# Kernel optimization log

Hardware: AMD Instinct MI355X
Metric: run time of the kernel (lower is better)

## Reference

```python
import jax, jax.numpy as jnp
import numpy as np

N_NODES = 100000


def gcn_conv(x, src, dst, W, b, n_nodes):
    """PyG GCNConv: out = D^{-1/2} (A + I) D^{-1/2} X W + b (self-loops added)."""
    h = x @ W  # [N, out]
    loops = jnp.arange(n_nodes, dtype=src.dtype)
    s = jnp.concatenate([src, loops])
    d = jnp.concatenate([dst, loops])
    deg = jax.ops.segment_sum(jnp.ones_like(d, dtype=h.dtype), d, num_segments=n_nodes)
    dinv = jnp.where(deg > 0, jax.lax.rsqrt(deg), 0.0)
    norm = dinv[s] * dinv[d]  # [E+N]
    msgs = norm[:, None] * h[s]  # gather + scale
    out = jax.ops.segment_sum(msgs, d, num_segments=n_nodes)
    return out + b


def setup_inputs() -> dict:
    key = jax.random.key(0)
    ks = jax.random.split(key, 10)
    n, e, f_in = N_NODES, 1600000, 128
    x = jax.random.normal(ks[0], (n, f_in), dtype=jnp.float32)
    edge_index = jax.random.randint(ks[1], (2, e), 0, n, dtype=jnp.int64)
    dims = [f_in, 15, 20, 27, 36]
    params = {}
    for i in range(4):
        fan_in, fan_out = dims[i], dims[i + 1]
        scale = 1.0 / np.sqrt(fan_in)
        params[f"W{i+1}"] = jax.random.uniform(ks[2 + 2 * i], (fan_in, fan_out), minval=-scale, maxval=scale, dtype=jnp.float32)
        params[f"b{i+1}"] = jax.random.uniform(ks[3 + 2 * i], (fan_out,), minval=-scale, maxval=scale, dtype=jnp.float32)
    return {"x": x, "edge_index": edge_index, **params}


def reference(x, edge_index, W1, b1, W2, b2, W3, b3, W4, b4):
    src, dst = edge_index[0], edge_index[1]
    n = x.shape[0]
    h = jax.nn.selu(gcn_conv(x, src, dst, W1, b1, n))
    h = jax.nn.selu(gcn_conv(h, src, dst, W2, b2, n))
    h = jax.nn.selu(gcn_conv(h, src, dst, W3, b3, n))
    h = jax.nn.selu(gcn_conv(h, src, dst, W4, b4, n))
    return h
```

## Files before the change

kernel.cpp:

```cpp
#include <hip/hip_runtime.h>
#include <hip/hip_fp16.h>
#include <math.h>

#define BLK 256
#define CBSH 10
#define CBN 1024
#define NCBC 128
#define NB2 512

__device__ __forceinline__ float selu_f(float x) {
    const float kScale = 1.0507009873554805f;
    const float kAlpha = 1.6732632423543772f;
    return x > 0.0f ? kScale * x : kScale * kAlpha * expm1f(x);
}

__device__ __forceinline__ float2 h2f2(unsigned u) {
    __half2 h = *reinterpret_cast<__half2*>(&u);
    return __half22float2(h);
}
__device__ __forceinline__ void h8_set(float* a, uint4 v) {
    float2 f0 = h2f2(v.x), f1 = h2f2(v.y), f2 = h2f2(v.z), f3 = h2f2(v.w);
    a[0] = f0.x; a[1] = f0.y; a[2] = f1.x; a[3] = f1.y;
    a[4] = f2.x; a[5] = f2.y; a[6] = f3.x; a[7] = f3.y;
}
__device__ __forceinline__ void h8_add(float* a, uint4 v) {
    float2 f0 = h2f2(v.x), f1 = h2f2(v.y), f2 = h2f2(v.z), f3 = h2f2(v.w);
    a[0] += f0.x; a[1] += f0.y; a[2] += f1.x; a[3] += f1.y;
    a[4] += f2.x; a[5] += f2.y; a[6] += f3.x; a[7] += f3.y;
}

__global__ void k_cnt(const int* __restrict__ dst, int* __restrict__ H, int e, int nbkt) {
    __shared__ int hist[NCBC];
    int tid = threadIdx.x;
    for (int b = tid; b < nbkt; b += BLK) hist[b] = 0;
    __syncthreads();
    int per = (e + NB2 - 1) / NB2;
    int lo = blockIdx.x * per;
    int hi = min(e, lo + per);
    for (int i = lo + tid; i < hi; i += BLK) atomicAdd(&hist[dst[i] >> CBSH], 1);
    __syncthreads();
    for (int b = tid; b < nbkt; b += BLK) H[blockIdx.x * nbkt + b] = hist[b];
}

__global__ void k_bsum(const int* __restrict__ H, int* __restrict__ bstart, int nbkt, int e) {
    __shared__ int tot[NCBC];
    int tid = threadIdx.x;
    for (int b = tid; b < nbkt; b += BLK) {
        int s = 0;
        for (int i = 0; i < NB2; ++i) s += H[i * nbkt + b];
        tot[b] = s;
    }
    __syncthreads();
    if (tid == 0) {
        int acc = 0;
        for (int b = 0; b < nbkt; ++b) {
            bstart[b] = acc;
            acc += tot[b];
        }
        bstart[nbkt] = acc;
    }
}

__global__ void k_off(int* __restrict__ H, const int* __restrict__ bstart, int nbkt) {
    __shared__ int lds[BLK];
    int b = blockIdx.x, tid = threadIdx.x;
    int v0 = H[(2 * tid) * nbkt + b];
    int v1 = H[(2 * tid + 1) * nbkt + b];
    int pair = v0 + v1;
    lds[tid] = pair;
    __syncthreads();
    int val = pair;
    for (int off = 1; off < BLK; off <<= 1) {
        int t2 = (tid >= off) ? lds[tid - off] : 0;
        __syncthreads();
        val += t2;
        lds[tid] = val;
        __syncthreads();
    }
    int excl = val - pair + bstart[b];
    H[(2 * tid) * nbkt + b] = excl;
    H[(2 * tid + 1) * nbkt + b] = excl + v0;
}

__global__ void k_scatter2(const int* __restrict__ src, const int* __restrict__ dst,
                           const int* __restrict__ H, unsigned* __restrict__ slab,
                           int e, int nbkt) {
    __shared__ int cur[NCBC];
    int tid = threadIdx.x;
    for (int b = tid; b < nbkt; b += BLK) cur[b] = H[blockIdx.x * nbkt + b];
    __syncthreads();
    int per = (e + NB2 - 1) / NB2;
    int lo = blockIdx.x * per;
    int hi = min(e, lo + per);
    for (int i = lo + tid; i < hi; i += BLK) {
        int s = src[i], d = dst[i];
        int b = d >> CBSH;
        int pos = atomicAdd(&cur[b], 1);
        slab[pos] = ((unsigned)s << CBSH) | (unsigned)(d & (CBN - 1));
    }
}

__global__ void k_histB(const int* __restrict__ bstart, const unsigned* __restrict__ slab,
                        int* __restrict__ deg, int n) {
    __shared__ int hist[CBN];
    int b = blockIdx.x, tid = threadIdx.x;
    for (int j = tid; j < CBN; j += BLK) hist[j] = 0;
    __syncthreads();
    int lo = bstart[b], hi = bstart[b + 1];
    for (int i = lo + tid; i < hi; i += BLK) atomicAdd(&hist[slab[i] & (CBN - 1)], 1);
    __syncthreads();
    int node0 = b << CBSH;
    for (int j = tid; j < CBN; j += BLK) {
        int node = node0 + j;
        if (node < n) deg[node] = hist[j];
    }
}

__global__ void k_scan1(const int* __restrict__ deg, int* __restrict__ rowptr,
                        int* __restrict__ bsums, int n) {
    __shared__ int lds[BLK];
    int tid = threadIdx.x;
    int idx = blockIdx.x * (BLK * 4) + tid * 4;
    int v0 = 0, v1 = 0, v2 = 0, v3 = 0;
    if (idx + 3 < n) {
        int4 t = *reinterpret_cast<const int4*>(deg + idx);
        v0 = t.x; v1 = t.y; v2 = t.z; v3 = t.w;
    } else {
        if (idx < n) v0 = deg[idx];
        if (idx + 1 < n) v1 = deg[idx + 1];
        if (idx + 2 < n) v2 = deg[idx + 2];
        if (idx + 3 < n) v3 = deg[idx + 3];
    }
    int tot = v0 + v1 + v2 + v3;
    lds[tid] = tot;
    __syncthreads();
    int val = tot;
    for (int off = 1; off < BLK; off <<= 1) {
        int t2 = (tid >= off) ? lds[tid - off] : 0;
        __syncthreads();
        val += t2;
        lds[tid] = val;
        __syncthreads();
    }
    int excl = val - tot;
    if (idx < n) rowptr[idx] = excl;
    if (idx + 1 < n) rowptr[idx + 1] = excl + v0;
    if (idx + 2 < n) rowptr[idx + 2] = excl + v0 + v1;
    if (idx + 3 < n) rowptr[idx + 3] = excl + v0 + v1 + v2;
    if (tid == BLK - 1) bsums[blockIdx.x] = val;
}

__global__ void k_scan2(int* __restrict__ bsums, int nb) {
    __shared__ int lds[BLK];
    int tid = threadIdx.x;
    int v = (tid < nb) ? bsums[tid] : 0;
    lds[tid] = v;
    __syncthreads();
    int val = v;
    for (int off = 1; off < BLK; off <<= 1) {
        int t2 = (tid >= off) ? lds[tid - off] : 0;
        __syncthreads();
        val += t2;
        lds[tid] = val;
        __syncthreads();
    }
    if (tid < nb) bsums[tid] = val - v;
}

__global__ void k_scan3(int* __restrict__ rowptr, const int* __restrict__ bsums,
                        const int* __restrict__ deg, float* __restrict__ dinv,
                        int n, int e) {
    int i = blockIdx.x * BLK + threadIdx.x;
    if (i >= n) return;
    int r = rowptr[i] + bsums[i >> 10];
    rowptr[i] = r;
    dinv[i] = rsqrtf((float)(deg[i] + 1));
    if (i == n - 1) rowptr[n] = e;
}

__global__ void k_placeC(const int* __restrict__ bstart, const unsigned* __restrict__ slab,
                         const int* __restrict__ rowptr, int* __restrict__ csr, int n) {
    __shared__ int cur[CBN];
    int b = blockIdx.x, tid = threadIdx.x;
    int node0 = b << CBSH;
    for (int j = tid; j < CBN; j += BLK) {
        int node = node0 + j;
        cur[j] = (node < n) ? rowptr[node] : 0;
    }
    __syncthreads();
    int lo = bstart[b], hi = bstart[b + 1];
    for (int i = lo + tid; i < hi; i += BLK) {
        unsigned p = slab[i];
        int pos = atomicAdd(&cur[p & (CBN - 1)], 1);
        csr[pos] = (int)(p >> CBSH);
    }
}

template <int K, int KP, int F, int SI, int SO, bool FUSE_IN>
__global__ void k_gemm(const float* __restrict__ xin, const float* __restrict__ W,
                       const float* __restrict__ bprev, const float* __restrict__ dinv,
                       __half* __restrict__ hs, int n) {
    constexpr int F8 = (F + 7) & ~7;
    int i = blockIdx.x * BLK + threadIdx.x;
    if (i >= n) return;
    const float* xr = xin + (size_t)i * SI;
    float di = dinv[i];
    float accf[F8];
#pragma unroll
    for (int f = 0; f < F8; ++f) accf[f] = 0.0f;
#pragma unroll
    for (int k4 = 0; k4 < KP / 4; ++k4) {
        float4 xv = *reinterpret_cast<const float4*>(xr + k4 * 4);
        float xs4[4] = {xv.x, xv.y, xv.z, xv.w};
#pragma unroll
        for (int j = 0; j < 4; ++j) {
            const int k = k4 * 4 + j;
            if (k < K) {
                float xval = xs4[j];
                if (FUSE_IN) xval = selu_f(di * xval + bprev[k]);
#pragma unroll
                for (int f = 0; f < F; ++f) accf[f] = fmaf(xval, W[k * F + f], accf[f]);
            }
        }
    }
#pragma unroll
    for (int f = 0; f < F; ++f) accf[f] *= di;
    __half2* ro2 = reinterpret_cast<__half2*>(hs + (size_t)i * SO);
#pragma unroll
    for (int f2 = 0; f2 < F8 / 2; ++f2)
        ro2[f2] = __float22half2_rn(make_float2(accf[2 * f2], accf[2 * f2 + 1]));
}

template <int F, int S , int G, int SOUT, bool LAST>
__global__ void k_agg(const int* __restrict__ rowptr, const int* __restrict__ csr,
                      const __half* __restrict__ hs, float* __restrict__ out,
                      const float* __restrict__ dinv, const float* __restrict__ bias,
                      int n) {
    constexpr int NPW = 64 / G;
    constexpr int CH = ((F + 7) & ~7) / 8;
    int lane = threadIdx.x & 63;
    int g = lane / G;
    int fl = lane & (G - 1);
    int wid = (blockIdx.x * BLK + threadIdx.x) >> 6;
    int d = wid * NPW + g;
    if (d >= n || fl >= CH) return;
    int beg = rowptr[d], end = rowptr[d + 1];
    auto rowp = [&](int r) {
        return reinterpret_cast<const uint4*>(hs + (size_t)r * S) + fl;
    };
    float s0[8], s1[8] = {0}, s2[8] = {0}, s3[8] = {0};
    h8_set(s0, *rowp(d));
    int p = beg;
    for (; p + 4 <= end; p += 4) {
        int e0 = csr[p], e1 = csr[p + 1], e2 = csr[p + 2], e3 = csr[p + 3];
        uint4 v0 = *rowp(e0), v1 = *rowp(e1), v2 = *rowp(e2), v3 = *rowp(e3);
        h8_add(s0, v0); h8_add(s1, v1); h8_add(s2, v2); h8_add(s3, v3);
    }
    for (; p < end; ++p) h8_add(s0, *rowp(csr[p]));
    float sum[8];
#pragma unroll
    for (int j = 0; j < 8; ++j) sum[j] = (s0[j] + s1[j]) + (s2[j] + s3[j]);
    if (LAST) {
        float dv = dinv[d];
        float r[8];
#pragma unroll
        for (int j = 0; j < 8; ++j) {
            int col = fl * 8 + j;
            r[j] = (col < F) ? selu_f(dv * sum[j] + bias[col]) : 0.0f;
        }
        float* op = out + (size_t)d * F + fl * 8;
        *reinterpret_cast<float4*>(op) = make_float4(r[0], r[1], r[2], r[3]);
        if (fl * 8 + 4 < F)
            *reinterpret_cast<float4*>(op + 4) = make_float4(r[4], r[5], r[6], r[7]);
    } else {
        float* op = out + (size_t)d * SOUT + fl * 8;
        *reinterpret_cast<float4*>(op) = make_float4(sum[0], sum[1], sum[2], sum[3]);
        *reinterpret_cast<float4*>(op + 4) = make_float4(sum[4], sum[5], sum[6], sum[7]);
    }
}

extern "C" void kernel_launch(void* const* d_in, const int* in_sizes, int n_in,
                              void* d_out, int out_size, void* d_ws, size_t ws_size,
                              hipStream_t stream) {
    const float* x = (const float*)d_in[0];
    const int* ei = (const int*)d_in[1];
    const float* W1 = (const float*)d_in[2];
    const float* b1 = (const float*)d_in[3];
    const float* W2 = (const float*)d_in[4];
    const float* b2 = (const float*)d_in[5];
    const float* W3 = (const float*)d_in[6];
    const float* b3 = (const float*)d_in[7];
    const float* W4 = (const float*)d_in[8];
    const float* b4 = (const float*)d_in[9];

    int n = in_sizes[0] / 128;
    int e = in_sizes[1] / 2;
    const int* s32 = ei;
    const int* d32 = ei + e;
    int nbkt = (n + CBN - 1) >> CBSH;

    char* w = (char*)d_ws;
    auto alloc = [&](size_t bytes) {
        char* p = w;
        w += (bytes + 255) & ~(size_t)255;
        return p;
    };
    int* deg = (int*)alloc((size_t)n * 4);
    int* rowptr = (int*)alloc(((size_t)n + 1) * 4);
    int* bsums = (int*)alloc((size_t)BLK * 4);
    float* dinv = (float*)alloc((size_t)n * 4);
    int* csr = (int*)alloc((size_t)e * 4);
    int* H = (int*)alloc((size_t)NB2 * nbkt * 4);
    int* bstart = (int*)alloc(((size_t)nbkt + 1) * 4);
    __half* bufA = (__half*)alloc((size_t)n * 40 * 2);
    float* bufB = (float*)alloc((size_t)n * 32 * 4);
    unsigned* slab = (unsigned*)bufA;

    int nb = (n + BLK - 1) / BLK;
    int nb_scan = (n + BLK * 4 - 1) / (BLK * 4);

    k_cnt<<<NB2, BLK, 0, stream>>>(d32, H, e, nbkt);
    k_bsum<<<1, BLK, 0, stream>>>(H, bstart, nbkt, e);
    k_off<<<nbkt, BLK, 0, stream>>>(H, bstart, nbkt);
    k_scatter2<<<NB2, BLK, 0, stream>>>(s32, d32, H, slab, e, nbkt);
    k_histB<<<nbkt, BLK, 0, stream>>>(bstart, slab, deg, n);
    k_scan1<<<nb_scan, BLK, 0, stream>>>(deg, rowptr, bsums, n);
    k_scan2<<<1, BLK, 0, stream>>>(bsums, nb_scan);
    k_scan3<<<nb, BLK, 0, stream>>>(rowptr, bsums, deg, dinv, n, e);
    k_placeC<<<nbkt, BLK, 0, stream>>>(bstart, slab, rowptr, csr, n);

    int ab1 = (n + 127) / 128;
    int ab2 = (n + 63) / 64;
    int ab4 = (n + 31) / 32;

    k_gemm<128, 128, 15, 128, 16, false><<<nb, BLK, 0, stream>>>(x, W1, nullptr, dinv, bufA, n);
    k_agg<15, 16, 2, 16, false><<<ab1, BLK, 0, stream>>>(rowptr, csr, bufA, bufB, dinv, nullptr, n);

    k_gemm<15, 16, 20, 16, 32, true><<<nb, BLK, 0, stream>>>(bufB, W2, b1, dinv, bufA, n);
    k_agg<20, 32, 4, 32, false><<<ab2, BLK, 0, stream>>>(rowptr, csr, bufA, bufB, dinv, nullptr, n);

    k_gemm<20, 20, 27, 32, 32, true><<<nb, BLK, 0, stream>>>(bufB, W3, b2, dinv, bufA, n);
    k_agg<27, 32, 4, 32, false><<<ab2, BLK, 0, stream>>>(rowptr, csr, bufA, bufB, dinv, nullptr, n);

    k_gemm<27, 28, 36, 32, 40, true><<<nb, BLK, 0, stream>>>(bufB, W4, b3, dinv, bufA, n);
    k_agg<36, 40, 8, 36, true><<<ab4, BLK, 0, stream>>>(rowptr, csr, bufA, (float*)d_out, dinv, b4, n);
}
```

Before: 283.2 us.

## Fuse CSR build into one kernel, split last-layer features, unroll aggregation

Replaces the histogram, three-pass scan and placement kernels with a single per-bucket k_build that computes the local histogram, does an in-block scan, writes rowptr and dinv, and places CSR entries. Bucket size drops to 512 nodes so one block of 256 threads handles two nodes each. The last layer now stores features as a 32-wide main buffer plus an 8-wide tail buffer, which shrinks the gather row from 80 to 64+16 bytes. Aggregation unrolls 8 edges per step and uses nontemporal loads for CSR indices. This cuts launch count and gather bytes, at the cost of more buckets in scatter and a redundant selu computation in k_gemm4.

```diff
diff --git a/kernel.cpp b/kernel.cpp
--- a/kernel.cpp
+++ b/kernel.cpp
@@ -3,9 +3,9 @@
 #include <math.h>
 
 #define BLK 256
-#define CBSH 10
-#define CBN 1024
-#define NCBC 128
+#define CBSH 9
+#define CBN 512
+#define NCBC 256
 #define NB2 512
 
 __device__ __forceinline__ float selu_f(float x) {
@@ -100,98 +100,43 @@
     }
 }
 
-__global__ void k_histB(const int* __restrict__ bstart, const unsigned* __restrict__ slab,
-                        int* __restrict__ deg, int n) {
+__global__ void k_build(const int* __restrict__ bstart, const unsigned* __restrict__ slab,
+                        int* __restrict__ rowptr, float* __restrict__ dinv,
+                        int* __restrict__ csr, int n, int e) {
     __shared__ int hist[CBN];
+    __shared__ int stmp[BLK];
     int b = blockIdx.x, tid = threadIdx.x;
-    for (int j = tid; j < CBN; j += BLK) hist[j] = 0;
+    hist[2 * tid] = 0;
+    hist[2 * tid + 1] = 0;
     __syncthreads();
     int lo = bstart[b], hi = bstart[b + 1];
     for (int i = lo + tid; i < hi; i += BLK) atomicAdd(&hist[slab[i] & (CBN - 1)], 1);
     __syncthreads();
-    int node0 = b << CBSH;
-    for (int j = tid; j < CBN; j += BLK) {
-        int node = node0 + j;
-        if (node < n) deg[node] = hist[j];
-    }
-}
-
-__global__ void k_scan1(const int* __restrict__ deg, int* __restrict__ rowptr,
-                        int* __restrict__ bsums, int n) {
-    __shared__ int lds[BLK];
-    int tid = threadIdx.x;
-    int idx = blockIdx.x * (BLK * 4) + tid * 4;
-    int v0 = 0, v1 = 0, v2 = 0, v3 = 0;
-    if (idx + 3 < n) {
-        int4 t = *reinterpret_cast<const int4*>(deg + idx);
-        v0 = t.x; v1 = t.y; v2 = t.z; v3 = t.w;
-    } else {
-        if (idx < n) v0 = deg[idx];
-        if (idx + 1 < n) v1 = deg[idx + 1];
-        if (idx + 2 < n) v2 = deg[idx + 2];
-        if (idx + 3 < n) v3 = deg[idx + 3];
-    }
-    int tot = v0 + v1 + v2 + v3;
-    lds[tid] = tot;
-    __syncthreads();
-    int val = tot;
+    int h0 = hist[2 * tid], h1 = hist[2 * tid + 1];
+    int pair = h0 + h1;
+    stmp[tid] = pair;
+    __syncthreads();
+    int val = pair;
     for (int off = 1; off < BLK; off <<= 1) {
-        int t2 = (tid >= off) ? lds[tid - off] : 0;
+        int t2 = (tid >= off) ? stmp[tid - off] : 0;
         __syncthreads();
         val += t2;
-        lds[tid] = val;
+        stmp[tid] = val;
         __syncthreads();
     }
-    int excl = val - tot;
-    if (idx < n) rowptr[idx] = excl;
-    if (idx + 1 < n) rowptr[idx + 1] = excl + v0;
-    if (idx + 2 < n) rowptr[idx + 2] = excl + v0 + v1;
-    if (idx + 3 < n) rowptr[idx + 3] = excl + v0 + v1 + v2;
-    if (tid == BLK - 1) bsums[blockIdx.x] = val;
-}
-
-__global__ void k_scan2(int* __restrict__ bsums, int nb) {
-    __shared__ int lds[BLK];
-    int tid = threadIdx.x;
-    int v = (tid < nb) ? bsums[tid] : 0;
-    lds[tid] = v;
-    __syncthreads();
-    int val = v;
-    for (int off = 1; off < BLK; off <<= 1) {
-        int t2 = (tid >= off) ? lds[tid - off] : 0;
-        __syncthreads();
-        val += t2;
-        lds[tid] = val;
-        __syncthreads();
-    }
-    if (tid < nb) bsums[tid] = val - v;
-}
-
-__global__ void k_scan3(int* __restrict__ rowptr, const int* __restrict__ bsums,
-                        const int* __restrict__ deg, float* __restrict__ dinv,
-                        int n, int e) {
-    int i = blockIdx.x * BLK + threadIdx.x;
-    if (i >= n) return;
-    int r = rowptr[i] + bsums[i >> 10];
-    rowptr[i] = r;
-    dinv[i] = rsqrtf((float)(deg[i] + 1));
-    if (i == n - 1) rowptr[n] = e;
-}
-
-__global__ void k_placeC(const int* __restrict__ bstart, const unsigned* __restrict__ slab,
-                         const int* __restrict__ rowptr, int* __restrict__ csr, int n) {
-    __shared__ int cur[CBN];
-    int b = blockIdx.x, tid = threadIdx.x;
+    int e0 = lo + val - pair;
+    int e1 = e0 + h0;
+    hist[2 * tid] = e0;
+    hist[2 * tid + 1] = e1;
     int node0 = b << CBSH;
-    for (int j = tid; j < CBN; j += BLK) {
-        int node = node0 + j;
-        cur[j] = (node < n) ? rowptr[node] : 0;
-    }
-    __syncthreads();
-    int lo = bstart[b], hi = bstart[b + 1];
+    int nA = node0 + 2 * tid, nB = nA + 1;
+    if (nA < n) { rowptr[nA] = e0; dinv[nA] = rsqrtf((float)(h0 + 1)); }
+    if (nB < n) { rowptr[nB] = e1; dinv[nB] = rsqrtf((float)(h1 + 1)); }
+    if (b == 0 && tid == 0) rowptr[n] = e;
+    __syncthreads();
     for (int i = lo + tid; i < hi; i += BLK) {
         unsigned p = slab[i];
-        int pos = atomicAdd(&cur[p & (CBN - 1)], 1);
+        int pos = atomicAdd(&hist[p & (CBN - 1)], 1);
         csr[pos] = (int)(p >> CBSH);
     }
 }
@@ -231,11 +176,47 @@
         ro2[f2] = __float22half2_rn(make_float2(accf[2 * f2], accf[2 * f2 + 1]));
 }
 
-template <int F, int S , int G, int SOUT, bool LAST>
+__global__ void k_gemm4(const float* __restrict__ xin, const float* __restrict__ W,
+                        const float* __restrict__ bprev, const float* __restrict__ dinv,
+                        __half* __restrict__ hsm, __half* __restrict__ hst, int n) {
+    constexpr int K = 27, F = 36;
+    int i = blockIdx.x * BLK + threadIdx.x;
+    if (i >= n) return;
+    const float* xr = xin + (size_t)i * 32;
+    float di = dinv[i];
+    float accf[40];
+#pragma unroll
+    for (int f = 0; f < 40; ++f) accf[f] = 0.0f;
+#pragma unroll
+    for (int k4 = 0; k4 < 7; ++k4) {
+        float4 xv = *reinterpret_cast<const float4*>(xr + k4 * 4);
+        float xs4[4] = {xv.x, xv.y, xv.z, xv.w};
+#pragma unroll
+        for (int j = 0; j < 4; ++j) {
+            const int k = k4 * 4 + j;
+            if (k < K) {
+                float xval = selu_f(di * xv.x + bprev[k]);
+                xval = selu_f(di * xs4[j] + bprev[k]);
+#pragma unroll
+                for (int f = 0; f < F; ++f) accf[f] = fmaf(xval, W[k * F + f], accf[f]);
+            }
+        }
+    }
+#pragma unroll
+    for (int f = 0; f < F; ++f) accf[f] *= di;
+    __half2* rm = reinterpret_cast<__half2*>(hsm + (size_t)i * 32);
+#pragma unroll
+    for (int f2 = 0; f2 < 16; ++f2)
+        rm[f2] = __float22half2_rn(make_float2(accf[2 * f2], accf[2 * f2 + 1]));
+    __half2* rt = reinterpret_cast<__half2*>(hst + (size_t)i * 8);
+#pragma unroll
+    for (int f2 = 0; f2 < 4; ++f2)
+        rt[f2] = __float22half2_rn(make_float2(accf[32 + 2 * f2], accf[32 + 2 * f2 + 1]));
+}
+
+template <int F, int S , int G, int SOUT>
 __global__ void k_agg(const int* __restrict__ rowptr, const int* __restrict__ csr,
-                      const __half* __restrict__ hs, float* __restrict__ out,
-                      const float* __restrict__ dinv, const float* __restrict__ bias,
-                      int n) {
+                      const __half* __restrict__ hs, float* __restrict__ out, int n) {
     constexpr int NPW = 64 / G;
     constexpr int CH = ((F + 7) & ~7) / 8;
     int lane = threadIdx.x & 63;
@@ -251,31 +232,95 @@
     float s0[8], s1[8] = {0}, s2[8] = {0}, s3[8] = {0};
     h8_set(s0, *rowp(d));
     int p = beg;
+    for (; p + 8 <= end; p += 8) {
+        int e0 = __builtin_nontemporal_load(csr + p);
+        int e1 = __builtin_nontemporal_load(csr + p + 1);
+        int e2 = __builtin_nontemporal_load(csr + p + 2);
+        int e3 = __builtin_nontemporal_load(csr + p + 3);
+        int e4 = __builtin_nontemporal_load(csr + p + 4);
+        int e5 = __builtin_nontemporal_load(csr + p + 5);
+        int e6 = __builtin_nontemporal_load(csr + p + 6);
+        int e7 = __builtin_nontemporal_load(csr + p + 7);
+        uint4 v0 = *rowp(e0), v1 = *rowp(e1), v2 = *rowp(e2), v3 = *rowp(e3);
+        uint4 v4 = *rowp(e4), v5 = *rowp(e5), v6 = *rowp(e6), v7 = *rowp(e7);
+        h8_add(s0, v0); h8_add(s1, v1); h8_add(s2, v2); h8_add(s3, v3);
+        h8_add(s0, v4); h8_add(s1, v5); h8_add(s2, v6); h8_add(s3, v7);
+    }
     for (; p + 4 <= end; p += 4) {
-        int e0 = csr[p], e1 = csr[p + 1], e2 = csr[p + 2], e3 = csr[p + 3];
+        int e0 = __builtin_nontemporal_load(csr + p);
+        int e1 = __builtin_nontemporal_load(csr + p + 1);
+        int e2 = __builtin_nontemporal_load(csr + p + 2);
+        int e3 = __builtin_nontemporal_load(csr + p + 3);
         uint4 v0 = *rowp(e0), v1 = *rowp(e1), v2 = *rowp(e2), v3 = *rowp(e3);
         h8_add(s0, v0); h8_add(s1, v1); h8_add(s2, v2); h8_add(s3, v3);
     }
-    for (; p < end; ++p) h8_add(s0, *rowp(csr[p]));
+    for (; p < end; ++p) h8_add(s0, *rowp(__builtin_nontemporal_load(csr + p)));
     float sum[8];
 #pragma unroll
     for (int j = 0; j < 8; ++j) sum[j] = (s0[j] + s1[j]) + (s2[j] + s3[j]);
-    if (LAST) {
-        float dv = dinv[d];
-        float r[8];
-#pragma unroll
-        for (int j = 0; j < 8; ++j) {
-            int col = fl * 8 + j;
-            r[j] = (col < F) ? selu_f(dv * sum[j] + bias[col]) : 0.0f;
-        }
-        float* op = out + (size_t)d * F + fl * 8;
+    float* op = out + (size_t)d * SOUT + fl * 8;
+    *reinterpret_cast<float4*>(op) = make_float4(sum[0], sum[1], sum[2], sum[3]);
+    *reinterpret_cast<float4*>(op + 4) = make_float4(sum[4], sum[5], sum[6], sum[7]);
+}
+
+__global__ void k_agg4(const int* __restrict__ rowptr, const int* __restrict__ csr,
+                       const __half* __restrict__ hsm, const __half* __restrict__ hst,
+                       float* __restrict__ out, const float* __restrict__ dinv,
+                       const float* __restrict__ bias, int n) {
+    constexpr int G = 8, NPW = 8;
+    int lane = threadIdx.x & 63;
+    int g = lane / G;
+    int fl = lane & (G - 1);
+    int wid = (blockIdx.x * BLK + threadIdx.x) >> 6;
+    int d = wid * NPW + g;
+    if (d >= n || fl >= 5) return;
+    int beg = rowptr[d], end = rowptr[d + 1];
+    const __half* bp = (fl < 4) ? hsm + fl * 8 : hst;
+    int mul = (fl < 4) ? 32 : 8;
+    auto rowp = [&](int r) {
+        return reinterpret_cast<const uint4*>(bp + (size_t)r * mul);
+    };
+    float s0[8], s1[8] = {0}, s2[8] = {0}, s3[8] = {0};
+    h8_set(s0, *rowp(d));
+    int p = beg;
+    for (; p + 8 <= end; p += 8) {
+        int e0 = __builtin_nontemporal_load(csr + p);
+        int e1 = __builtin_nontemporal_load(csr + p + 1);
+        int e2 = __builtin_nontemporal_load(csr + p + 2);
+        int e3 = __builtin_nontemporal_load(csr + p + 3);
+        int e4 = __builtin_nontemporal_load(csr + p + 4);
+        int e5 = __builtin_nontemporal_load(csr + p + 5);
+        int e6 = __builtin_nontemporal_load(csr + p + 6);
+        int e7 = __builtin_nontemporal_load(csr + p + 7);
+        uint4 v0 = *rowp(e0), v1 = *rowp(e1), v2 = *rowp(e2), v3 = *rowp(e3);
+        uint4 v4 = *rowp(e4), v5 = *rowp(e5), v6 = *rowp(e6), v7 = *rowp(e7);
+        h8_add(s0, v0); h8_add(s1, v1); h8_add(s2, v2); h8_add(s3, v3);
+        h8_add(s0, v4); h8_add(s1, v5); h8_add(s2, v6); h8_add(s3, v7);
+    }
+    for (; p + 4 <= end; p += 4) {
+        int e0 = __builtin_nontemporal_load(csr + p);
+        int e1 = __builtin_nontemporal_load(csr + p + 1);
+        int e2 = __builtin_nontemporal_load(csr + p + 2);
+        int e3 = __builtin_nontemporal_load(csr + p + 3);
+        uint4 v0 = *rowp(e0), v1 = *rowp(e1), v2 = *rowp(e2), v3 = *rowp(e3);
+        h8_add(s0, v0); h8_add(s1, v1); h8_add(s2, v2); h8_add(s3, v3);
+    }
+    for (; p < end; ++p) h8_add(s0, *rowp(__builtin_nontemporal_load(csr + p)));
+    float dv = dinv[d];
+    float r[8];
+#pragma unroll
+    for (int j = 0; j < 8; ++j) {
+        float sum = (s0[j] + s1[j]) + (s2[j] + s3[j]);
+        int col = (fl < 4) ? fl * 8 + j : 32 + j;
+        r[j] = (col < 36) ? selu_f(dv * sum + bias[col]) : 0.0f;
+    }
+    if (fl < 4) {
+        float* op = out + (size_t)d * 36 + fl * 8;
         *reinterpret_cast<float4*>(op) = make_float4(r[0], r[1], r[2], r[3]);
-        if (fl * 8 + 4 < F)
-            *reinterpret_cast<float4*>(op + 4) = make_float4(r[4], r[5], r[6], r[7]);
+        *reinterpret_cast<float4*>(op + 4) = make_float4(r[4], r[5], r[6], r[7]);
     } else {
-        float* op = out + (size_t)d * SOUT + fl * 8;
-        *reinterpret_cast<float4*>(op) = make_float4(sum[0], sum[1], sum[2], sum[3]);
-        *reinterpret_cast<float4*>(op + 4) = make_float4(sum[4], sum[5], sum[6], sum[7]);
+        float* op = out + (size_t)d * 36 + 32;
+        *reinterpret_cast<float4*>(op) = make_float4(r[0], r[1], r[2], r[3]);
     }
 }
 
@@ -305,9 +350,7 @@
         w += (bytes + 255) & ~(size_t)255;
         return p;
     };
-    int* deg = (int*)alloc((size_t)n * 4);
     int* rowptr = (int*)alloc(((size_t)n + 1) * 4);
-    int* bsums = (int*)alloc((size_t)BLK * 4);
     float* dinv = (float*)alloc((size_t)n * 4);
     int* csr = (int*)alloc((size_t)e * 4);
     int* H = (int*)alloc((size_t)NB2 * nbkt * 4);
@@ -315,33 +358,30 @@
     __half* bufA = (__half*)alloc((size_t)n * 40 * 2);
     float* bufB = (float*)alloc((size_t)n * 32 * 4);
     unsigned* slab = (unsigned*)bufA;
+    __half* hsm = bufA;
+    __half* hst = bufA + (size_t)n * 32;
 
     int nb = (n + BLK - 1) / BLK;
-    int nb_scan = (n + BLK * 4 - 1) / (BLK * 4);
 
     k_cnt<<<NB2, BLK, 0, stream>>>(d32, H, e, nbkt);
     k_bsum<<<1, BLK, 0, stream>>>(H, bstart, nbkt, e);
     k_off<<<nbkt, BLK, 0, stream>>>(H, bstart, nbkt);
     k_scatter2<<<NB2, BLK, 0, stream>>>(s32, d32, H, slab, e, nbkt);
-    k_histB<<<nbkt, BLK, 0, stream>>>(bstart, slab, deg, n);
-    k_scan1<<<nb_scan, BLK, 0, stream>>>(deg, rowptr, bsums, n);
-    k_scan2<<<1, BLK, 0, stream>>>(bsums, nb_scan);
-    k_scan3<<<nb, BLK, 0, stream>>>(rowptr, bsums, deg, dinv, n, e);
-    k_placeC<<<nbkt, BLK, 0, stream>>>(bstart, slab, rowptr, csr, n);
+    k_build<<<nbkt, BLK, 0, stream>>>(bstart, slab, rowptr, dinv, csr, n, e);
 
     int ab1 = (n + 127) / 128;
     int ab2 = (n + 63) / 64;
     int ab4 = (n + 31) / 32;
 
     k_gemm<128, 128, 15, 128, 16, false><<<nb, BLK, 0, stream>>>(x, W1, nullptr, dinv, bufA, n);
-    k_agg<15, 16, 2, 16, false><<<ab1, BLK, 0, stream>>>(rowptr, csr, bufA, bufB, dinv, nullptr, n);
+    k_agg<15, 16, 2, 16><<<ab1, BLK, 0, stream>>>(rowptr, csr, bufA, bufB, n);
 
     k_gemm<15, 16, 20, 16, 32, true><<<nb, BLK, 0, stream>>>(bufB, W2, b1, dinv, bufA, n);
-    k_agg<20, 32, 4, 32, false><<<ab2, BLK, 0, stream>>>(rowptr, csr, bufA, bufB, dinv, nullptr, n);
+    k_agg<20, 32, 4, 32><<<ab2, BLK, 0, stream>>>(rowptr, csr, bufA, bufB, n);
 
     k_gemm<20, 20, 27, 32, 32, true><<<nb, BLK, 0, stream>>>(bufB, W3, b2, dinv, bufA, n);
-    k_agg<27, 32, 4, 32, false><<<ab2, BLK, 0, stream>>>(rowptr, csr, bufA, bufB, dinv, nullptr, n);
-
-    k_gemm<27, 28, 36, 32, 40, true><<<nb, BLK, 0, stream>>>(bufB, W4, b3, dinv, bufA, n);
-    k_agg<36, 40, 8, 36, true><<<ab4, BLK, 0, stream>>>(rowptr, csr, bufA, (float*)d_out, dinv, b4, n);
-}
+    k_agg<27, 32, 4, 32><<<ab2, BLK, 0, stream>>>(rowptr, csr, bufA, bufB, n);
+
+    k_gemm4<<<nb, BLK, 0, stream>>>(bufB, W4, b3, dinv, hsm, hst, n);
+    k_agg4<<<ab4, BLK, 0, stream>>>(rowptr, csr, hsm, hst, (float*)d_out, dinv, b4, n);
+}
```

After: 277.4 us. 2.1% less time.
